# Performance work log

Measured on AMD Instinct MI355X. Metric: run time of the kernel, lower is better.

## Reference

```python
import jax, jax.numpy as jnp
import numpy as np
from jax import lax

WINDOW_SIZE = 11
SIGMA = 1.5
VAL_RANGE = 1.0  # L; val_range=1 passed at init
C2 = (0.03 * VAL_RANGE) ** 2


def _gaussian_window(channel):
    # 1D gaussian, normalized, then outer product -> 2D window, depthwise kernel
    x = jnp.arange(WINDOW_SIZE, dtype=jnp.float32) - WINDOW_SIZE // 2
    g = jnp.exp(-(x ** 2) / (2.0 * SIGMA ** 2))
    g = g / g.sum()
    w2d = jnp.outer(g, g)  # [11, 11]
    # OIHW depthwise kernel: [C, 1, 11, 11]
    return jnp.broadcast_to(w2d, (channel, 1, WINDOW_SIZE, WINDOW_SIZE))


def _dwconv(x, kernel, channel):
    pad = WINDOW_SIZE // 2
    return lax.conv_general_dilated(
        x, kernel, window_strides=(1, 1),
        padding=[(pad, pad), (pad, pad)],
        dimension_numbers=('NCHW', 'OIHW', 'NCHW'),
        feature_group_count=channel)


def setup_inputs() -> dict:
    key = jax.random.key(0)
    k1, k2 = jax.random.split(key)
    shape = (32, 3, 512, 512)
    img1 = jax.random.uniform(k1, shape, dtype=jnp.float32)
    img2 = jax.random.uniform(k2, shape, dtype=jnp.float32)
    return {"img1": img1, "img2": img2}


def reference(img1, img2):
    channel = img1.shape[1]
    kernel = _gaussian_window(channel)
    mu1 = _dwconv(img1, kernel, channel)
    mu2 = _dwconv(img2, kernel, channel)
    mu1_mu2 = mu1 * mu2
    sigma1_sq = _dwconv(img1 * img1, kernel, channel) - mu1 * mu1
    sigma2_sq = _dwconv(img2 * img2, kernel, channel) - mu2 * mu2
    sigma12 = _dwconv(img1 * img2, kernel, channel) - mu1_mu2
    sigma1 = jnp.sqrt(jnp.abs(sigma1_sq))
    sigma2 = jnp.sqrt(jnp.abs(sigma2_sq))
    ss_map = (sigma12 + C2) / (sigma1 * sigma2 + C2)
    return ss_map.mean()  # size_average=True
```

## Files before the change

kernel.cpp:

```cpp
#include <hip/hip_runtime.h>
#include <hip/hip_bf16.h>

#define WIN 11
#define PAD 5
#define TW 32
#define TH 64
#define IH 74
#define ISTR 52
#define NCHK 12
#define HSTR 33
#define IMG_H 512
#define IMG_W 512
#define BLK 512

__global__ __launch_bounds__(BLK, 4) void ssim_main(const float* __restrict__ img1,
                                                    const float* __restrict__ img2,
                                                    float* __restrict__ partial) {
    __shared__ float  lx[IH * ISTR];
    __shared__ float  ly[IH * ISTR];
    __shared__ float4 h4[IH * HSTR];
    __shared__ float  h1[IH * HSTR];
    __shared__ float  wsum[8];

    const int tid = threadIdx.x;
    const int tx0 = blockIdx.x * TW;
    const int ty0 = blockIdx.y * TH;
    const size_t base = (size_t)blockIdx.z * (size_t)(IMG_H * IMG_W);

    float g[WIN];
    {
        float s = 0.f;
#pragma unroll
        for (int i = 0; i < WIN; ++i) {
            float d = (float)(i - PAD);
            g[i] = expf(-d * d / 4.5f);
            s += g[i];
        }
        float inv = 1.f / s;
#pragma unroll
        for (int i = 0; i < WIN; ++i) g[i] *= inv;
    }

    const bool interior = (blockIdx.x >= 1) & (blockIdx.x <= 14) &
                          (blockIdx.y >= 1) & (blockIdx.y <= (IMG_H / TH - 2));
    if (interior) {
        for (int t = tid; t < IH * NCHK; t += BLK) {
            int r = t / NCHK, k = t - r * NCHK;
            const size_t off = base + (size_t)(ty0 + r - PAD) * IMG_W + (tx0 - 8 + 4 * k);
            *(float4*)(lx + r * ISTR + 4 * k) = *(const float4*)(img1 + off);
            *(float4*)(ly + r * ISTR + 4 * k) = *(const float4*)(img2 + off);
        }
    } else {
        for (int t = tid; t < IH * NCHK; t += BLK) {
            int r = t / NCHK, k = t - r * NCHK;
            int gr = ty0 + r - PAD;
            int gc0 = tx0 - 8 + 4 * k;
            float4 a = make_float4(0.f, 0.f, 0.f, 0.f);
            float4 b = make_float4(0.f, 0.f, 0.f, 0.f);
            if (gr >= 0 && gr < IMG_H) {
                const size_t rowoff = base + (size_t)gr * IMG_W;
                if (gc0 >= 0 && gc0 + 3 < IMG_W) {
                    a = *(const float4*)(img1 + rowoff + gc0);
                    b = *(const float4*)(img2 + rowoff + gc0);
                } else {
                    a.x = (gc0 + 0 >= 0 && gc0 + 0 < IMG_W) ? img1[rowoff + gc0 + 0] : 0.f;
                    a.y = (gc0 + 1 >= 0 && gc0 + 1 < IMG_W) ? img1[rowoff + gc0 + 1] : 0.f;
                    a.z = (gc0 + 2 >= 0 && gc0 + 2 < IMG_W) ? img1[rowoff + gc0 + 2] : 0.f;
                    a.w = (gc0 + 3 >= 0 && gc0 + 3 < IMG_W) ? img1[rowoff + gc0 + 3] : 0.f;
                    b.x = (gc0 + 0 >= 0 && gc0 + 0 < IMG_W) ? img2[rowoff + gc0 + 0] : 0.f;
                    b.y = (gc0 + 1 >= 0 && gc0 + 1 < IMG_W) ? img2[rowoff + gc0 + 1] : 0.f;
                    b.z = (gc0 + 2 >= 0 && gc0 + 2 < IMG_W) ? img2[rowoff + gc0 + 2] : 0.f;
                    b.w = (gc0 + 3 >= 0 && gc0 + 3 < IMG_W) ? img2[rowoff + gc0 + 3] : 0.f;
                }
            }
            *(float4*)(lx + r * ISTR + 4 * k) = a;
            *(float4*)(ly + r * ISTR + 4 * k) = b;
        }
    }
    __syncthreads();

    for (int t = tid; t < IH * 8 + 48; t += BLK) {
        int c0g = (t >> 3) & 7;
        int r = (t & 7) + ((t >> 6) << 3);
        if (r < IH) {
            float ax[20], bx[20];
#pragma unroll
            for (int j = 0; j < 5; ++j) {
                float4 va = *(const float4*)(lx + r * ISTR + 4 * (c0g + j));
                float4 vb = *(const float4*)(ly + r * ISTR + 4 * (c0g + j));
                ax[4 * j + 0] = va.x; ax[4 * j + 1] = va.y; ax[4 * j + 2] = va.z; ax[4 * j + 3] = va.w;
                bx[4 * j + 0] = vb.x; bx[4 * j + 1] = vb.y; bx[4 * j + 2] = vb.z; bx[4 * j + 3] = vb.w;
            }
#pragma unroll
            for (int cc = 0; cc < 4; ++cc) {
                float sx = 0.f, sy = 0.f, sxx = 0.f, syy = 0.f, sxy = 0.f;
#pragma unroll
                for (int j = 0; j < WIN; ++j) {
                    float w = g[j];
                    float a = ax[cc + 3 + j];
                    float b = bx[cc + 3 + j];
                    float wa = w * a, wb = w * b;
                    sx += wa;
                    sy += wb;
                    sxx = fmaf(wa, a, sxx);
                    syy = fmaf(wb, b, syy);
                    sxy = fmaf(wa, b, sxy);
                }
                int o = r * HSTR + 4 * c0g + cc;
                h4[o] = make_float4(sx, sy, sxx, syy);
                h1[o] = sxy;
            }
        }
    }
    __syncthreads();

    const float C2v = 0.0009f;
    float acc = 0.f;
    {
        int c = tid & 31;
        int r0 = (tid >> 5) * 4;
        float vsx[4] = {0.f, 0.f, 0.f, 0.f};
        float vsy[4] = {0.f, 0.f, 0.f, 0.f};
        float vxx[4] = {0.f, 0.f, 0.f, 0.f};
        float vyy[4] = {0.f, 0.f, 0.f, 0.f};
        float vxy[4] = {0.f, 0.f, 0.f, 0.f};
#pragma unroll
        for (int i = 0; i < WIN + 3; ++i) {
            float4 h = h4[(r0 + i) * HSTR + c];
            float  e = h1[(r0 + i) * HSTR + c];
#pragma unroll
            for (int k = 0; k < 4; ++k) {
                if (i >= k && i <= k + 10) {
                    float w = g[i - k];
                    vsx[k] = fmaf(w, h.x, vsx[k]);
                    vsy[k] = fmaf(w, h.y, vsy[k]);
                    vxx[k] = fmaf(w, h.z, vxx[k]);
                    vyy[k] = fmaf(w, h.w, vyy[k]);
                    vxy[k] = fmaf(w, e,  vxy[k]);
                }
            }
        }
#pragma unroll
        for (int k = 0; k < 4; ++k) {
            float mu12 = vsx[k] * vsy[k];
            float s1 = vxx[k] - vsx[k] * vsx[k];
            float s2 = vyy[k] - vsy[k] * vsy[k];
            float s12 = vxy[k] - mu12;
            float sig = sqrtf(fabsf(s1)) * sqrtf(fabsf(s2));
            acc += (s12 + C2v) / (sig + C2v);
        }
    }

#pragma unroll
    for (int off = 32; off > 0; off >>= 1) acc += __shfl_down(acc, off, 64);
    int wave = tid >> 6;
    if ((tid & 63) == 0) wsum[wave] = acc;
    __syncthreads();
    if (tid == 0) {
        float b = 0.f;
#pragma unroll
        for (int w = 0; w < BLK / 64; ++w) b += wsum[w];
        int bid = (blockIdx.z * gridDim.y + blockIdx.y) * gridDim.x + blockIdx.x;
        partial[bid] = b;
    }
}

__global__ __launch_bounds__(1024) void ssim_final(const float* __restrict__ partial,
                                                   int n, float* __restrict__ out,
                                                   double inv_total) {
    __shared__ double wsd[16];
    double s = 0.0;
    const float4* p4 = (const float4*)partial;
    for (int i = threadIdx.x; i < n / 4; i += 1024) {
        float4 v = p4[i];
        s += (double)v.x + (double)v.y + (double)v.z + (double)v.w;
    }
#pragma unroll
    for (int off = 32; off > 0; off >>= 1) s += __shfl_down(s, off, 64);
    int wave = threadIdx.x >> 6;
    if ((threadIdx.x & 63) == 0) wsd[wave] = s;
    __syncthreads();
    if (threadIdx.x == 0) {
        double t = 0.0;
#pragma unroll
        for (int w = 0; w < 16; ++w) t += wsd[w];
        out[0] = (float)(t * inv_total);
    }
}

extern "C" void kernel_launch(void* const* d_in, const int* in_sizes, int n_in,
                              void* d_out, int out_size, void* d_ws, size_t ws_size,
                              hipStream_t stream) {
    const float* img1 = (const float*)d_in[0];
    const float* img2 = (const float*)d_in[1];
    float* out = (float*)d_out;
    float* partial = (float*)d_ws;

    const int total = in_sizes[0];
    const int nc = total / (IMG_H * IMG_W);

    dim3 grid(IMG_W / TW, IMG_H / TH, nc);
    const int nblocks = grid.x * grid.y * grid.z;

    ssim_main<<<grid, BLK, 0, stream>>>(img1, img2, partial);
    ssim_final<<<1, 1024, 0, stream>>>(partial, nblocks, out, 1.0 / (double)total);
}
```

Baseline: 302.2 us.

## Load input halo directly from global into registers, dropping LDS staging

Removes the shared-memory staging buffers for both images and the barrier after them. Each horizontal-pass thread now reads its 20-wide row segment straight from global memory as float4 loads, with per-chunk zero-fill at the borders. The smaller LDS footprint allows the launch-bounds occupancy hint to rise from 4 to 6 blocks. In exchange, overlapping column chunks are re-read from global/L2 by neighbouring threads, which adds redundant memory traffic.

Result: slower. 711.3 us (+135.4%).

```diff
diff --git a/kernel.cpp b/kernel.cpp
--- a/kernel.cpp
+++ b/kernel.cpp
@@ -6,18 +6,14 @@
 #define TW 32
 #define TH 64
 #define IH 74
-#define ISTR 52
-#define NCHK 12
 #define HSTR 33
 #define IMG_H 512
 #define IMG_W 512
 #define BLK 512
 
-__global__ __launch_bounds__(BLK, 4) void ssim_main(const float* __restrict__ img1,
+__global__ __launch_bounds__(BLK, 6) void ssim_main(const float* __restrict__ img1,
                                                     const float* __restrict__ img2,
                                                     float* __restrict__ partial) {
-    __shared__ float  lx[IH * ISTR];
-    __shared__ float  ly[IH * ISTR];
     __shared__ float4 h4[IH * HSTR];
     __shared__ float  h1[IH * HSTR];
     __shared__ float  wsum[8];
@@ -41,55 +37,40 @@
         for (int i = 0; i < WIN; ++i) g[i] *= inv;
     }
 
-    const bool interior = (blockIdx.x >= 1) & (blockIdx.x <= 14) &
+    const bool interior = (blockIdx.x >= 1) & (blockIdx.x <= (IMG_W / TW - 2)) &
                           (blockIdx.y >= 1) & (blockIdx.y <= (IMG_H / TH - 2));
-    if (interior) {
-        for (int t = tid; t < IH * NCHK; t += BLK) {
-            int r = t / NCHK, k = t - r * NCHK;
-            const size_t off = base + (size_t)(ty0 + r - PAD) * IMG_W + (tx0 - 8 + 4 * k);
-            *(float4*)(lx + r * ISTR + 4 * k) = *(const float4*)(img1 + off);
-            *(float4*)(ly + r * ISTR + 4 * k) = *(const float4*)(img2 + off);
-        }
-    } else {
-        for (int t = tid; t < IH * NCHK; t += BLK) {
-            int r = t / NCHK, k = t - r * NCHK;
-            int gr = ty0 + r - PAD;
-            int gc0 = tx0 - 8 + 4 * k;
-            float4 a = make_float4(0.f, 0.f, 0.f, 0.f);
-            float4 b = make_float4(0.f, 0.f, 0.f, 0.f);
-            if (gr >= 0 && gr < IMG_H) {
-                const size_t rowoff = base + (size_t)gr * IMG_W;
-                if (gc0 >= 0 && gc0 + 3 < IMG_W) {
-                    a = *(const float4*)(img1 + rowoff + gc0);
-                    b = *(const float4*)(img2 + rowoff + gc0);
-                } else {
-                    a.x = (gc0 + 0 >= 0 && gc0 + 0 < IMG_W) ? img1[rowoff + gc0 + 0] : 0.f;
-                    a.y = (gc0 + 1 >= 0 && gc0 + 1 < IMG_W) ? img1[rowoff + gc0 + 1] : 0.f;
-                    a.z = (gc0 + 2 >= 0 && gc0 + 2 < IMG_W) ? img1[rowoff + gc0 + 2] : 0.f;
-                    a.w = (gc0 + 3 >= 0 && gc0 + 3 < IMG_W) ? img1[rowoff + gc0 + 3] : 0.f;
-                    b.x = (gc0 + 0 >= 0 && gc0 + 0 < IMG_W) ? img2[rowoff + gc0 + 0] : 0.f;
-                    b.y = (gc0 + 1 >= 0 && gc0 + 1 < IMG_W) ? img2[rowoff + gc0 + 1] : 0.f;
-                    b.z = (gc0 + 2 >= 0 && gc0 + 2 < IMG_W) ? img2[rowoff + gc0 + 2] : 0.f;
-                    b.w = (gc0 + 3 >= 0 && gc0 + 3 < IMG_W) ? img2[rowoff + gc0 + 3] : 0.f;
-                }
-            }
-            *(float4*)(lx + r * ISTR + 4 * k) = a;
-            *(float4*)(ly + r * ISTR + 4 * k) = b;
-        }
-    }
-    __syncthreads();
 
     for (int t = tid; t < IH * 8 + 48; t += BLK) {
         int c0g = (t >> 3) & 7;
         int r = (t & 7) + ((t >> 6) << 3);
         if (r < IH) {
+            int gr = ty0 + r - PAD;
             float ax[20], bx[20];
+            if (interior) {
+                const float* q1 = img1 + base + (size_t)gr * IMG_W + (tx0 - 8 + 4 * c0g);
+                const float* q2 = img2 + base + (size_t)gr * IMG_W + (tx0 - 8 + 4 * c0g);
 #pragma unroll
-            for (int j = 0; j < 5; ++j) {
-                float4 va = *(const float4*)(lx + r * ISTR + 4 * (c0g + j));
-                float4 vb = *(const float4*)(ly + r * ISTR + 4 * (c0g + j));
-                ax[4 * j + 0] = va.x; ax[4 * j + 1] = va.y; ax[4 * j + 2] = va.z; ax[4 * j + 3] = va.w;
-                bx[4 * j + 0] = vb.x; bx[4 * j + 1] = vb.y; bx[4 * j + 2] = vb.z; bx[4 * j + 3] = vb.w;
+                for (int j = 0; j < 5; ++j) {
+                    float4 va = *(const float4*)(q1 + 4 * j);
+                    float4 vb = *(const float4*)(q2 + 4 * j);
+                    ax[4 * j + 0] = va.x; ax[4 * j + 1] = va.y; ax[4 * j + 2] = va.z; ax[4 * j + 3] = va.w;
+                    bx[4 * j + 0] = vb.x; bx[4 * j + 1] = vb.y; bx[4 * j + 2] = vb.z; bx[4 * j + 3] = vb.w;
+                }
+            } else {
+                const bool rowok = (unsigned)gr < (unsigned)IMG_H;
+                const size_t rowoff = base + (size_t)(rowok ? gr : 0) * IMG_W;
+#pragma unroll
+                for (int j = 0; j < 5; ++j) {
+                    int gc = tx0 - 8 + 4 * (c0g + j);
+                    float4 va = make_float4(0.f, 0.f, 0.f, 0.f);
+                    float4 vb = make_float4(0.f, 0.f, 0.f, 0.f);
+                    if (rowok && (unsigned)gc < (unsigned)IMG_W) {
+                        va = *(const float4*)(img1 + rowoff + gc);
+                        vb = *(const float4*)(img2 + rowoff + gc);
+                    }
+                    ax[4 * j + 0] = va.x; ax[4 * j + 1] = va.y; ax[4 * j + 2] = va.z; ax[4 * j + 3] = va.w;
+                    bx[4 * j + 0] = vb.x; bx[4 * j + 1] = vb.y; bx[4 * j + 2] = vb.z; bx[4 * j + 3] = vb.w;
+                }
             }
 #pragma unroll
             for (int cc = 0; cc < 4; ++cc) {
```
